# Optimization experiments

Hardware: AMD Instinct MI355X
Metric: run time of the kernel (lower is better)

## Reference

```python
import jax, jax.numpy as jnp
import numpy as np

EPS = 1e-7  # Keras K.epsilon()
ROUTINGS = 3

def squash(v, axis=-1):
    s2 = jnp.sum(jnp.square(v), axis=axis, keepdims=True)
    scale = s2 / (1.0 + s2) / jnp.sqrt(s2 + EPS)
    return scale * v

def setup_inputs() -> dict:
    key = jax.random.key(0)
    k1, k2 = jax.random.split(key)
    B, IN_CAPS, IN_DIM = 64, 2048, 8
    NUM_CAPS, DIM = 32, 16
    inputs = jax.random.normal(k1, (B, IN_CAPS, IN_DIM), dtype=jnp.float32)
    W = jax.random.normal(k2, (NUM_CAPS, IN_CAPS, DIM, IN_DIM), dtype=jnp.float32) * 0.05
    return {"inputs": inputs, "W": W}

def reference(inputs, W):
    # inputs: [B, I, Di]; W: [N, I, Do, Di]
    # inputs_hat[b,n,i,do] = sum_di inputs[b,i,di] * W[n,i,do,di]
    inputs_hat = jnp.einsum('bid,nied->bnie', inputs, W)  # [B, N, I, Do]
    B, N, I, Do = inputs_hat.shape
    b = jnp.zeros((B, N, I), dtype=inputs_hat.dtype)
    outputs = None
    for r in range(ROUTINGS):
        c = jax.nn.softmax(b, axis=1)                       # over num_capsule
        s = jnp.einsum('bni,bnie->bne', c, inputs_hat)      # [B, N, Do]
        outputs = squash(s)
        if r < ROUTINGS - 1:
            b = b + jnp.einsum('bne,bnie->bni', outputs, inputs_hat)
    return outputs
```

## Files before the change

### kernel.cpp

```cpp
#include <hip/hip_runtime.h>


#define BATCH  64
#define NCAPS  32
#define ICAPS  2048
#define DI     8
#define DOUT   16
#define NPW    4
#define NWAVES 8
#define THREADS 512
#define NBLK   256
#define ICH    8
#define WTILE  (NCAPS * DOUT * DI)
#define SSLICE (NCAPS * BATCH * DOUT)

__device__ __forceinline__ void glds16(const float* g, float* l) {
    __builtin_amdgcn_global_load_lds(
        (const __attribute__((address_space(1))) void*)g,
        (__attribute__((address_space(3))) void*)l, 16, 0, 0);
}

template<int MODE>
__global__ __launch_bounds__(THREADS, 2)
void caps_iter(const float* __restrict__ X, const float* __restrict__ Wg,
               const float* __restrict__ Oprev, float* __restrict__ Pout)
{
    __shared__ float Wl[2][WTILE];
    __shared__ float4 Xa[ICH][BATCH];
    __shared__ float4 Xb[ICH][BATCH];
    __shared__ float red[2][NWAVES][64];

    const int t    = threadIdx.x;
    const int lane = t & 63;
    const int wu   = __builtin_amdgcn_readfirstlane(t >> 6);
    const int i0   = blockIdx.x * ICH;

    {
        const int b = t >> 3, c = t & 7;
        const float* xp = X + ((size_t)b * ICAPS + i0 + c) * DI;
        Xa[c][b] = *(const float4*)xp;
        Xb[c][b] = *(const float4*)(xp + 4);
    }

    float oreg[NPW][DOUT];
    if constexpr (MODE) {
        #pragma unroll
        for (int nn = 0; nn < NPW; ++nn) {
            const float* op = Oprev + ((size_t)(wu * NPW + nn) * BATCH + lane) * DOUT;
            #pragma unroll
            for (int q = 0; q < 4; ++q) {
                const float4 v = *(const float4*)(op + q * 4);
                oreg[nn][q*4+0] = v.x; oreg[nn][q*4+1] = v.y;
                oreg[nn][q*4+2] = v.z; oreg[nn][q*4+3] = v.w;
            }
        }
    }

    float sacc[NPW][DOUT];
    #pragma unroll
    for (int nn = 0; nn < NPW; ++nn)
        #pragma unroll
        for (int e = 0; e < DOUT; ++e) sacc[nn][e] = 0.f;

    auto stage = [&](float* dst, int i_) {
        #pragma unroll
        for (int r = 0; r < 2; ++r) {
            const int f   = r * THREADS + t;
            const int n_  = f >> 5;
            const int off = f & 31;
            const float* g = Wg + ((size_t)n_ * ICAPS + i_) * (DOUT * DI) + off * 4;
            glds16(g, dst + f * 4);
        }
    };

    stage(&Wl[0][0], i0);
    asm volatile("s_waitcnt lgkmcnt(0)\n\ts_barrier" ::: "memory");

    for (int ii = 0; ii < ICH; ++ii) {
        const int cur = ii & 1;
        if (ii + 1 < ICH) {
            stage(&Wl[cur ^ 1][0], i0 + ii + 1);
            asm volatile("s_waitcnt vmcnt(2)\n\ts_barrier" ::: "memory");
        } else {
            asm volatile("s_waitcnt vmcnt(0)\n\ts_barrier" ::: "memory");
        }

        float xv[DI];
        {
            const float4 va = Xa[ii][lane];
            const float4 vb = Xb[ii][lane];
            xv[0]=va.x; xv[1]=va.y; xv[2]=va.z; xv[3]=va.w;
            xv[4]=vb.x; xv[5]=vb.y; xv[6]=vb.z; xv[7]=vb.w;
        }

        float hat[NPW][DOUT];
        float logit[NPW];
        #pragma unroll
        for (int nn = 0; nn < NPW; ++nn) {
            const float* Wp = &Wl[cur][(wu * NPW + nn) * (DOUT * DI)];
            float lg = 0.f;
            #pragma unroll
            for (int e = 0; e < DOUT; ++e) {
                const float4 wa = *(const float4*)(Wp + e * DI);
                const float4 wb = *(const float4*)(Wp + e * DI + 4);
                float h = wa.x * xv[0];
                h = fmaf(wa.y, xv[1], h); h = fmaf(wa.z, xv[2], h);
                h = fmaf(wa.w, xv[3], h); h = fmaf(wb.x, xv[4], h);
                h = fmaf(wb.y, xv[5], h); h = fmaf(wb.z, xv[6], h);
                h = fmaf(wb.w, xv[7], h);
                hat[nn][e] = h;
                if constexpr (MODE) lg = fmaf(oreg[nn][e], h, lg);
            }
            logit[nn] = lg;
        }

        float c[NPW];
        if constexpr (MODE) {
            const float m4 = fmaxf(fmaxf(logit[0], logit[1]), fmaxf(logit[2], logit[3]));
            red[0][wu][lane] = m4;
            asm volatile("s_waitcnt lgkmcnt(0)\n\ts_barrier" ::: "memory");
            float M = red[0][0][lane];
            #pragma unroll
            for (int w2 = 1; w2 < NWAVES; ++w2) M = fmaxf(M, red[0][w2][lane]);
            float sum4 = 0.f;
            #pragma unroll
            for (int nn = 0; nn < NPW; ++nn) { c[nn] = __expf(logit[nn] - M); sum4 += c[nn]; }
            red[1][wu][lane] = sum4;
            asm volatile("s_waitcnt lgkmcnt(0)\n\ts_barrier" ::: "memory");
            float den = 0.f;
            #pragma unroll
            for (int w2 = 0; w2 < NWAVES; ++w2) den += red[1][w2][lane];
            const float rden = 1.0f / den;
            #pragma unroll
            for (int nn = 0; nn < NPW; ++nn) c[nn] *= rden;
        }

        #pragma unroll
        for (int nn = 0; nn < NPW; ++nn) {
            const float cc = MODE ? c[nn] : 0.03125f;
            #pragma unroll
            for (int e = 0; e < DOUT; ++e)
                sacc[nn][e] = fmaf(cc, hat[nn][e], sacc[nn][e]);
        }

        if constexpr (!MODE) {
            asm volatile("s_waitcnt lgkmcnt(0)\n\ts_barrier" ::: "memory");
        }
    }

    float* P = Pout + (size_t)blockIdx.x * SSLICE;
    #pragma unroll
    for (int nn = 0; nn < NPW; ++nn) {
        float* p = P + ((size_t)(wu * NPW + nn) * BATCH + lane) * DOUT;
        #pragma unroll
        for (int q = 0; q < 4; ++q) {
            float4 v;
            v.x = sacc[nn][q*4+0]; v.y = sacc[nn][q*4+1];
            v.z = sacc[nn][q*4+2]; v.w = sacc[nn][q*4+3];
            *(float4*)(p + q * 4) = v;
        }
    }
}

template<int STEP>
__global__ __launch_bounds__(512)
void caps_rs(const float* __restrict__ P, float* __restrict__ Obuf,
             float* __restrict__ Out)
{
    const int t  = threadIdx.x;
    const int e  = t & 15;
    const int bl = (t >> 4) & 7;
    const int h  = t >> 7;
    const int n  = blockIdx.x >> 3;
    const int bg = blockIdx.x & 7;
    const int b  = bg * 8 + bl;

    const float* p0 = P + (size_t)(h * 64) * SSLICE + ((size_t)n * BATCH + b) * DOUT + e;
    float a0 = 0.f, a1 = 0.f, a2 = 0.f, a3 = 0.f;
    for (int k = 0; k < 64; k += 4) {
        a0 += p0[(size_t)(k + 0) * SSLICE];
        a1 += p0[(size_t)(k + 1) * SSLICE];
        a2 += p0[(size_t)(k + 2) * SSLICE];
        a3 += p0[(size_t)(k + 3) * SSLICE];
    }
    const float acc = (a0 + a1) + (a2 + a3);

    __shared__ float sh[4][128];
    sh[h][(bl << 4) | e] = acc;
    __syncthreads();

    if (t < 128) {
        const float v = sh[0][t] + sh[1][t] + sh[2][t] + sh[3][t];
        float v2 = v * v;
        #pragma unroll
        for (int m = 1; m < 16; m <<= 1) v2 += __shfl_xor(v2, m, 16);
        const float scale = v2 / ((1.f + v2) * sqrtf(v2 + 1e-7f));
        const float val = scale * v;
        const size_t oidx = ((size_t)n * BATCH + b) * DOUT + e;
        if constexpr (STEP == 0)      Obuf[oidx] = val;
        else if constexpr (STEP == 1) Obuf[oidx] += val;
        else Out[((size_t)b * NCAPS + n) * DOUT + e] = val;
    }
}

extern "C" void kernel_launch(void* const* d_in, const int* in_sizes, int n_in,
                              void* d_out, int out_size, void* d_ws, size_t ws_size,
                              hipStream_t stream)
{
    (void)in_sizes; (void)n_in; (void)out_size; (void)ws_size;
    const float* X = (const float*)d_in[0];
    const float* W = (const float*)d_in[1];
    float* out  = (float*)d_out;
    float* obuf = (float*)d_ws;
    float* part = obuf + SSLICE;

    const dim3 gI(NBLK), bI(THREADS), gR(NBLK), bR(512);

    caps_iter<0><<<gI, bI, 0, stream>>>(X, W, nullptr, part);
    caps_rs  <0><<<gR, bR, 0, stream>>>(part, obuf, out);
    caps_iter<1><<<gI, bI, 0, stream>>>(X, W, obuf, part);
    caps_rs  <1><<<gR, bR, 0, stream>>>(part, obuf, out);
    caps_iter<1><<<gI, bI, 0, stream>>>(X, W, obuf, part);
    caps_rs  <2><<<gR, bR, 0, stream>>>(part, obuf, out);
}
```

Before: 224.4 us.

## Remap threads to capsules with shuffle softmax and padded W layout

Reassigns caps_iter threads so each lane owns one output capsule and four batches. The routing softmax over capsules then runs as intra-wave shuffles instead of LDS reductions with block barriers. W is prefetched through registers into a padded float2 shared layout, and x values are reused across four batches per weight read. The partial-sum layout becomes batch-major, so the reduce kernel uses coalesced float4 loads and writes the output directly. In exchange it adds register pressure and drops the asynchronous global-to-LDS copies.

```diff
diff --git a/kernel.cpp b/kernel.cpp
--- a/kernel.cpp
+++ b/kernel.cpp
@@ -1,163 +1,169 @@
 #include <hip/hip_runtime.h>
 
 
-#define BATCH  64
-#define NCAPS  32
-#define ICAPS  2048
-#define DI     8
-#define DOUT   16
-#define NPW    4
-#define NWAVES 8
+#define BATCH   64
+#define NCAPS   32
+#define ICAPS   2048
+#define DI      8
+#define DOUT    16
 #define THREADS 512
-#define NBLK   256
-#define ICH    8
-#define WTILE  (NCAPS * DOUT * DI)
-#define SSLICE (NCAPS * BATCH * DOUT)
-
-__device__ __forceinline__ void glds16(const float* g, float* l) {
-    __builtin_amdgcn_global_load_lds(
-        (const __attribute__((address_space(1))) void*)g,
-        (__attribute__((address_space(3))) void*)l, 16, 0, 0);
-}
+#define NBLK    256
+#define ICH     8
+#define WROWS   64
+#define WPAD    33
+#define SSLICE  (NCAPS * BATCH * DOUT)
 
 template<int MODE>
 __global__ __launch_bounds__(THREADS, 2)
 void caps_iter(const float* __restrict__ X, const float* __restrict__ Wg,
                const float* __restrict__ Oprev, float* __restrict__ Pout)
 {
-    __shared__ float Wl[2][WTILE];
-    __shared__ float4 Xa[ICH][BATCH];
-    __shared__ float4 Xb[ICH][BATCH];
-    __shared__ float red[2][NWAVES][64];
-
-    const int t    = threadIdx.x;
-    const int lane = t & 63;
-    const int wu   = __builtin_amdgcn_readfirstlane(t >> 6);
-    const int i0   = blockIdx.x * ICH;
-
-    {
-        const int b = t >> 3, c = t & 7;
-        const float* xp = X + ((size_t)b * ICAPS + i0 + c) * DI;
-        Xa[c][b] = *(const float4*)xp;
-        Xb[c][b] = *(const float4*)(xp + 4);
-    }
-
-    float oreg[NPW][DOUT];
+    __shared__ float2 Wl[2][WROWS * WPAD];
+    __shared__ float  Xs[ICH][BATCH * DI];
+
+    const int t  = threadIdx.x;
+    const int n  = t & 31;
+    const int b4 = t >> 5;
+    const int b0 = b4 * 4;
+    const int i0 = blockIdx.x * ICH;
+
+    const int sn = t >> 4;
+    const int se = t & 15;
+    const float* wsrc = Wg + ((size_t)sn * ICAPS + i0) * (DOUT * DI) + se * DI;
+
+    float o[4][DOUT];
     if constexpr (MODE) {
         #pragma unroll
-        for (int nn = 0; nn < NPW; ++nn) {
-            const float* op = Oprev + ((size_t)(wu * NPW + nn) * BATCH + lane) * DOUT;
+        for (int j = 0; j < 4; ++j) {
+            const float* op = Oprev + ((size_t)(b0 + j) * NCAPS + n) * DOUT;
             #pragma unroll
             for (int q = 0; q < 4; ++q) {
                 const float4 v = *(const float4*)(op + q * 4);
-                oreg[nn][q*4+0] = v.x; oreg[nn][q*4+1] = v.y;
-                oreg[nn][q*4+2] = v.z; oreg[nn][q*4+3] = v.w;
-            }
-        }
-    }
-
-    float sacc[NPW][DOUT];
+                o[j][q*4+0] = v.x; o[j][q*4+1] = v.y;
+                o[j][q*4+2] = v.z; o[j][q*4+3] = v.w;
+            }
+        }
+    }
+
+    float4 wr0, wr1;
+    {
+        const int xb = t >> 3, xi = t & 7;
+        const float* xp = X + ((size_t)xb * ICAPS + i0 + xi) * DI;
+        const float4 xa = *(const float4*)xp;
+        const float4 xc = *(const float4*)(xp + 4);
+        wr0 = *(const float4*)(wsrc);
+        wr1 = *(const float4*)(wsrc + 4);
+        *(float4*)&Xs[xi][xb * DI]     = xa;
+        *(float4*)&Xs[xi][xb * DI + 4] = xc;
+        float2* wd = &Wl[0][0];
+        wd[(se*4+0)*WPAD + sn] = make_float2(wr0.x, wr0.y);
+        wd[(se*4+1)*WPAD + sn] = make_float2(wr0.z, wr0.w);
+        wd[(se*4+2)*WPAD + sn] = make_float2(wr1.x, wr1.y);
+        wd[(se*4+3)*WPAD + sn] = make_float2(wr1.z, wr1.w);
+    }
+    __syncthreads();
+
+    float sacc[4][DOUT];
     #pragma unroll
-    for (int nn = 0; nn < NPW; ++nn)
-        #pragma unroll
-        for (int e = 0; e < DOUT; ++e) sacc[nn][e] = 0.f;
-
-    auto stage = [&](float* dst, int i_) {
-        #pragma unroll
-        for (int r = 0; r < 2; ++r) {
-            const int f   = r * THREADS + t;
-            const int n_  = f >> 5;
-            const int off = f & 31;
-            const float* g = Wg + ((size_t)n_ * ICAPS + i_) * (DOUT * DI) + off * 4;
-            glds16(g, dst + f * 4);
-        }
-    };
-
-    stage(&Wl[0][0], i0);
-    asm volatile("s_waitcnt lgkmcnt(0)\n\ts_barrier" ::: "memory");
-
+    for (int j = 0; j < 4; ++j)
+        #pragma unroll
+        for (int e = 0; e < DOUT; ++e) sacc[j][e] = 0.f;
+
+    #pragma unroll 1
     for (int ii = 0; ii < ICH; ++ii) {
-        const int cur = ii & 1;
-        if (ii + 1 < ICH) {
-            stage(&Wl[cur ^ 1][0], i0 + ii + 1);
-            asm volatile("s_waitcnt vmcnt(2)\n\ts_barrier" ::: "memory");
-        } else {
-            asm volatile("s_waitcnt vmcnt(0)\n\ts_barrier" ::: "memory");
-        }
-
-        float xv[DI];
+        const float2* wcur = &Wl[ii & 1][0];
+        float2*       wnxt = &Wl[(ii & 1) ^ 1][0];
+        const bool pre = (ii + 1 < ICH);
+        if (pre) {
+            const float* ws = wsrc + (size_t)(ii + 1) * (DOUT * DI);
+            wr0 = *(const float4*)ws;
+            wr1 = *(const float4*)(ws + 4);
+        }
+
+        float hat[4][DOUT];
+        float logit[4] = {0.f, 0.f, 0.f, 0.f};
+
         {
-            const float4 va = Xa[ii][lane];
-            const float4 vb = Xb[ii][lane];
-            xv[0]=va.x; xv[1]=va.y; xv[2]=va.z; xv[3]=va.w;
-            xv[4]=vb.x; xv[5]=vb.y; xv[6]=vb.z; xv[7]=vb.w;
-        }
-
-        float hat[NPW][DOUT];
-        float logit[NPW];
-        #pragma unroll
-        for (int nn = 0; nn < NPW; ++nn) {
-            const float* Wp = &Wl[cur][(wu * NPW + nn) * (DOUT * DI)];
-            float lg = 0.f;
+            float4 xh[4];
+            #pragma unroll
+            for (int j = 0; j < 4; ++j)
+                xh[j] = *(const float4*)&Xs[ii][(b0 + j) * DI];
             #pragma unroll
             for (int e = 0; e < DOUT; ++e) {
-                const float4 wa = *(const float4*)(Wp + e * DI);
-                const float4 wb = *(const float4*)(Wp + e * DI + 4);
-                float h = wa.x * xv[0];
-                h = fmaf(wa.y, xv[1], h); h = fmaf(wa.z, xv[2], h);
-                h = fmaf(wa.w, xv[3], h); h = fmaf(wb.x, xv[4], h);
-                h = fmaf(wb.y, xv[5], h); h = fmaf(wb.z, xv[6], h);
-                h = fmaf(wb.w, xv[7], h);
-                hat[nn][e] = h;
-                if constexpr (MODE) lg = fmaf(oreg[nn][e], h, lg);
-            }
-            logit[nn] = lg;
-        }
-
-        float c[NPW];
+                const float2 wA = wcur[(e*4+0)*WPAD + n];
+                const float2 wB = wcur[(e*4+1)*WPAD + n];
+                #pragma unroll
+                for (int j = 0; j < 4; ++j) {
+                    float h =       wA.x * xh[j].x;
+                    h = fmaf(wA.y, xh[j].y, h);
+                    h = fmaf(wB.x, xh[j].z, h);
+                    h = fmaf(wB.y, xh[j].w, h);
+                    hat[j][e] = h;
+                }
+            }
+        }
+        {
+            float4 xh[4];
+            #pragma unroll
+            for (int j = 0; j < 4; ++j)
+                xh[j] = *(const float4*)&Xs[ii][(b0 + j) * DI + 4];
+            #pragma unroll
+            for (int e = 0; e < DOUT; ++e) {
+                const float2 wC = wcur[(e*4+2)*WPAD + n];
+                const float2 wD = wcur[(e*4+3)*WPAD + n];
+                #pragma unroll
+                for (int j = 0; j < 4; ++j) {
+                    float h = hat[j][e];
+                    h = fmaf(wC.x, xh[j].x, h);
+                    h = fmaf(wC.y, xh[j].y, h);
+                    h = fmaf(wD.x, xh[j].z, h);
+                    h = fmaf(wD.y, xh[j].w, h);
+                    hat[j][e] = h;
+                    if constexpr (MODE) logit[j] = fmaf(o[j][e], h, logit[j]);
+                }
+            }
+        }
+
+        float c[4];
         if constexpr (MODE) {
-            const float m4 = fmaxf(fmaxf(logit[0], logit[1]), fmaxf(logit[2], logit[3]));
-            red[0][wu][lane] = m4;
-            asm volatile("s_waitcnt lgkmcnt(0)\n\ts_barrier" ::: "memory");
-            float M = red[0][0][lane];
-            #pragma unroll
-            for (int w2 = 1; w2 < NWAVES; ++w2) M = fmaxf(M, red[0][w2][lane]);
-            float sum4 = 0.f;
-            #pragma unroll
-            for (int nn = 0; nn < NPW; ++nn) { c[nn] = __expf(logit[nn] - M); sum4 += c[nn]; }
-            red[1][wu][lane] = sum4;
-            asm volatile("s_waitcnt lgkmcnt(0)\n\ts_barrier" ::: "memory");
-            float den = 0.f;
-            #pragma unroll
-            for (int w2 = 0; w2 < NWAVES; ++w2) den += red[1][w2][lane];
-            const float rden = 1.0f / den;
-            #pragma unroll
-            for (int nn = 0; nn < NPW; ++nn) c[nn] *= rden;
-        }
-
-        #pragma unroll
-        for (int nn = 0; nn < NPW; ++nn) {
-            const float cc = MODE ? c[nn] : 0.03125f;
+            #pragma unroll
+            for (int j = 0; j < 4; ++j) {
+                float M = logit[j];
+                #pragma unroll
+                for (int m = 1; m < 32; m <<= 1) M = fmaxf(M, __shfl_xor(M, m));
+                const float ex = __expf(logit[j] - M);
+                float den = ex;
+                #pragma unroll
+                for (int m = 1; m < 32; m <<= 1) den += __shfl_xor(den, m);
+                c[j] = ex / den;
+            }
+        }
+
+        #pragma unroll
+        for (int j = 0; j < 4; ++j) {
+            const float cc = MODE ? c[j] : 0.03125f;
             #pragma unroll
             for (int e = 0; e < DOUT; ++e)
-                sacc[nn][e] = fmaf(cc, hat[nn][e], sacc[nn][e]);
-        }
-
-        if constexpr (!MODE) {
-            asm volatile("s_waitcnt lgkmcnt(0)\n\ts_barrier" ::: "memory");
-        }
+                sacc[j][e] = fmaf(cc, hat[j][e], sacc[j][e]);
+        }
+
+        if (pre) {
+            wnxt[(se*4+0)*WPAD + sn] = make_float2(wr0.x, wr0.y);
+            wnxt[(se*4+1)*WPAD + sn] = make_float2(wr0.z, wr0.w);
+            wnxt[(se*4+2)*WPAD + sn] = make_float2(wr1.x, wr1.y);
+            wnxt[(se*4+3)*WPAD + sn] = make_float2(wr1.z, wr1.w);
+        }
+        __syncthreads();
     }
 
     float* P = Pout + (size_t)blockIdx.x * SSLICE;
     #pragma unroll
-    for (int nn = 0; nn < NPW; ++nn) {
-        float* p = P + ((size_t)(wu * NPW + nn) * BATCH + lane) * DOUT;
+    for (int j = 0; j < 4; ++j) {
+        float* p = P + ((size_t)(b0 + j) * NCAPS + n) * DOUT;
         #pragma unroll
         for (int q = 0; q < 4; ++q) {
-            float4 v;
-            v.x = sacc[nn][q*4+0]; v.y = sacc[nn][q*4+1];
-            v.z = sacc[nn][q*4+2]; v.w = sacc[nn][q*4+3];
-            *(float4*)(p + q * 4) = v;
+            *(float4*)(p + q * 4) = make_float4(sacc[j][q*4+0], sacc[j][q*4+1],
+                                                sacc[j][q*4+2], sacc[j][q*4+3]);
         }
     }
 }
@@ -167,39 +173,32 @@
 void caps_rs(const float* __restrict__ P, float* __restrict__ Obuf,
              float* __restrict__ Out)
 {
-    const int t  = threadIdx.x;
-    const int e  = t & 15;
-    const int bl = (t >> 4) & 7;
-    const int h  = t >> 7;
-    const int n  = blockIdx.x >> 3;
-    const int bg = blockIdx.x & 7;
-    const int b  = bg * 8 + bl;
-
-    const float* p0 = P + (size_t)(h * 64) * SSLICE + ((size_t)n * BATCH + b) * DOUT + e;
-    float a0 = 0.f, a1 = 0.f, a2 = 0.f, a3 = 0.f;
-    for (int k = 0; k < 64; k += 4) {
-        a0 += p0[(size_t)(k + 0) * SSLICE];
-        a1 += p0[(size_t)(k + 1) * SSLICE];
-        a2 += p0[(size_t)(k + 2) * SSLICE];
-        a3 += p0[(size_t)(k + 3) * SSLICE];
-    }
-    const float acc = (a0 + a1) + (a2 + a3);
-
-    __shared__ float sh[4][128];
-    sh[h][(bl << 4) | e] = acc;
+    __shared__ float sh[16][128];
+    const int t = threadIdx.x, g = blockIdx.x;
+    const int kq = t >> 5, j = t & 31;
+    const int base = g * 128;
+    const float* p = P + base + j * 4;
+    float4 a = make_float4(0.f, 0.f, 0.f, 0.f);
+    #pragma unroll
+    for (int kk = 0; kk < 16; ++kk) {
+        const float4 v = *(const float4*)(p + (size_t)(kq * 16 + kk) * SSLICE);
+        a.x += v.x; a.y += v.y; a.z += v.z; a.w += v.w;
+    }
+    *(float4*)&sh[kq][j * 4] = a;
     __syncthreads();
-
     if (t < 128) {
-        const float v = sh[0][t] + sh[1][t] + sh[2][t] + sh[3][t];
+        float v = 0.f;
+        #pragma unroll
+        for (int q = 0; q < 16; ++q) v += sh[q][t];
         float v2 = v * v;
         #pragma unroll
-        for (int m = 1; m < 16; m <<= 1) v2 += __shfl_xor(v2, m, 16);
+        for (int m = 1; m < 16; m <<= 1) v2 += __shfl_xor(v2, m);
         const float scale = v2 / ((1.f + v2) * sqrtf(v2 + 1e-7f));
         const float val = scale * v;
-        const size_t oidx = ((size_t)n * BATCH + b) * DOUT + e;
-        if constexpr (STEP == 0)      Obuf[oidx] = val;
-        else if constexpr (STEP == 1) Obuf[oidx] += val;
-        else Out[((size_t)b * NCAPS + n) * DOUT + e] = val;
+        const int f = base + t;
+        if constexpr (STEP == 0)      Obuf[f] = val;
+        else if constexpr (STEP == 1) Obuf[f] += val;
+        else                          Out[f]  = val;
     }
 }
 
```

After: 223.1 us. No clear change (-0.6%).
